# Kernel tuning notes

Measured on AMD Instinct MI355X. Metric: run time of the kernel, lower is better.

## Reference

```python
import jax, jax.numpy as jnp
import numpy as np

INPUT_DIM = 512
LATENT_DIM = 64
H1, H2 = 128, 64  # hardcoded hidden widths in Encoder/Decoder
BATCH = 4096


def _xavier(key, shape):
    fan_out, fan_in = shape
    std = jnp.sqrt(2.0 / (fan_in + fan_out))
    return std * jax.random.normal(key, shape, dtype=jnp.float32)


def setup_inputs() -> dict:
    key = jax.random.key(0)
    ks = jax.random.split(key, 10)
    d = LATENT_DIM
    n_pairs = d * (d - 1) // 2
    n_funcs = 1 + d + n_pairs  # bias + states + pairwise products
    inp = {
        "x": jax.random.normal(ks[0], (BATCH, INPUT_DIM), dtype=jnp.float32),
        "xdot": jax.random.normal(ks[1], (BATCH, INPUT_DIM), dtype=jnp.float32),
        # encoder weights (torch Linear layout: [out, in])
        "We1": _xavier(ks[2], (H1, INPUT_DIM)), "be1": jnp.zeros((H1,), jnp.float32),
        "We2": _xavier(ks[3], (H2, H1)),        "be2": jnp.zeros((H2,), jnp.float32),
        "We3": _xavier(ks[4], (d, H2)),         "be3": jnp.zeros((d,), jnp.float32),
        # decoder weights
        "Wd1": _xavier(ks[5], (H2, d)),         "bd1": jnp.zeros((H2,), jnp.float32),
        "Wd2": _xavier(ks[6], (H1, H2)),        "bd2": jnp.zeros((H1,), jnp.float32),
        "Wd3": _xavier(ks[7], (INPUT_DIM, H1)), "bd3": jnp.zeros((INPUT_DIM,), jnp.float32),
        "XI": jnp.ones((n_funcs, d), jnp.float32),
        "XI_mask": jnp.ones((n_funcs, d), jnp.float32),
    }
    return inp


def _mlp_with_jacobian(x, Ws, bs):
    """3-layer relu MLP; returns output and per-sample analytic Jacobian [B,out,in].
    Jacobian = diag(m3) W3 diag(m2) W2 diag(m1) W1 with relu masks m_l."""
    h = x
    J = None
    for W, b in zip(Ws, bs):
        h = h @ W.T + b                      # [B, out_l]
        m = (h > 0).astype(h.dtype)          # relu mask (grad 0 at 0, matching torch)
        h = jnp.maximum(h, 0)
        Wm = m[:, :, None] * W[None]         # [B, out_l, in_l]
        J = Wm if J is None else jnp.einsum('boh,bhi->boi', Wm, J)
    return h, J


def _sindy_library(z):
    B, d = z.shape
    iu, ju = np.triu_indices(d, k=1)
    ones = jnp.ones((B, 1), z.dtype)
    pairs = z[:, iu] * z[:, ju]              # [B, d(d-1)/2]
    return jnp.concatenate([ones, z, pairs], axis=1)


def reference(x, xdot, We1, be1, We2, be2, We3, be3,
              Wd1, bd1, Wd2, bd2, Wd3, bd3, XI, XI_mask):
    z, Jenc = _mlp_with_jacobian(x, (We1, We2, We3), (be1, be2, be3))
    dz_dt = jnp.einsum('bli,bi->bl', Jenc, xdot)
    xh, Jdec = _mlp_with_jacobian(z, (Wd1, Wd2, Wd3), (bd1, bd2, bd3))
    theta = _sindy_library(z)
    dz_dt_sindy = theta @ (XI_mask * XI)
    dxh_dt = jnp.einsum('bol,bl->bo', Jdec, dz_dt_sindy)
    return (xh, dxh_dt, z, dz_dt, dz_dt_sindy)
```

## Files before the change

kernel.cpp:

```cpp
#include <hip/hip_runtime.h>

#define BATCH 4096
#define IN_DIM 512
#define H1DIM 128
#define H2DIM 64
#define DDIM 64
#define NFUNC 2081
#define NFPAD 2112
#define CHUNK 704
#define KS_PER_CHUNK 22

typedef short bf16x8 __attribute__((ext_vector_type(8)));
typedef float f32x4 __attribute__((ext_vector_type(4)));
#define MFMA(a,b,c) __builtin_amdgcn_mfma_f32_16x16x32_bf16(a,b,c,0,0,0)

#define WSZ1 (H1DIM*IN_DIM)
#define WSZ2 (H2DIM*H1DIM)
#define WSZ3 (DDIM*H2DIM)
#define WSZ4 (H2DIM*DDIM)
#define WSZ5 (H1DIM*H2DIM)
#define WSZ6 (IN_DIM*H1DIM)

__device__ __forceinline__ short f2b(float f) {
    union { float f; unsigned u; } x; x.f = f;
    unsigned r = x.u + 0x7fffu + ((x.u >> 16) & 1u);
    return (short)(r >> 16);
}
__device__ __forceinline__ float b2f(short s) {
    union { unsigned u; float f; } x; x.u = ((unsigned)(unsigned short)s) << 16;
    return x.f;
}
__device__ __forceinline__ void split3f(float v, short& s0, short& s1, short& s2) {
    s0 = f2b(v); float r = v - b2f(s0);
    s1 = f2b(r); float r2 = r - b2f(s1);
    s2 = f2b(r2);
}

__device__ __forceinline__ void st_b16(short* t, int RS, int r, int c, short v) {
    int b = (c * 2) ^ ((r & 7) << 4);
    *(short*)((char*)(t + r * RS) + b) = v;
}
__device__ __forceinline__ void st_b32s(short* t, int RS, int r, int c, unsigned v) {
    int b = (c * 2) ^ ((r & 7) << 4);
    *(unsigned*)((char*)(t + r * RS) + b) = v;
}
__device__ __forceinline__ bf16x8 ld_af(const short* t, int RS, int lane, int kbase) {
    int r = lane & 15;
    int b = ((kbase + (lane >> 4) * 8) * 2) ^ ((r & 7) << 4);
    return *(const bf16x8*)((const char*)(t + r * RS) + b);
}
__device__ __forceinline__ bf16x8 ld_bp(const short* P, int blk, int lane) {
    return *(const bf16x8*)(P + ((size_t)blk * 64 + lane) * 8);
}

__device__ __forceinline__ void mf9(bf16x8 f0, bf16x8 f1, bf16x8 f2, bf16x8 fv,
                                    bf16x8 b0, bf16x8 b1, bf16x8 b2,
                                    f32x4& P, f32x4& Q, f32x4& V) {
    P = MFMA(f0, b0, P); Q = MFMA(f1, b1, Q);
    P = MFMA(f1, b0, P); Q = MFMA(f0, b1, Q);
    P = MFMA(f2, b0, P); Q = MFMA(f2, b1, Q);
    P = MFMA(f0, b2, P); Q = MFMA(f1, b2, Q);
    V = MFMA(fv, b0, V);
}

__device__ __forceinline__ void epi_store(short* t0, short* t1, short* t2, short* tv, int RS,
                                          int lane, int col, const f32x4& P, const f32x4& Q,
                                          const f32x4& V, float bb)
{
    #pragma unroll
    for (int q = 0; q < 4; ++q) {
        int row = (lane >> 4) * 4 + q;
        float pre = P[q] + Q[q] + bb;
        float h = fmaxf(pre, 0.f);
        short s0, s1, s2;
        split3f(h, s0, s1, s2);
        st_b16(t0, RS, row, col, s0);
        st_b16(t1, RS, row, col, s1);
        st_b16(t2, RS, row, col, s2);
        st_b16(tv, RS, row, col, pre > 0.f ? f2b(V[q]) : (short)0);
    }
}

template<int K>
__device__ void pack_w(const float* __restrict__ W, short* __restrict__ dst, int NK,
                       int gid, int nthr)
{
    for (int o = gid; o < NK / 8; o += nthr) {
        int c = o / (K / 8), k0 = (o - c * (K / 8)) * 8;
        int cb = c >> 4, ks = k0 >> 5;
        int L = (((k0 >> 3) & 3) << 4) | (c & 15);
        int idx = ((cb * (K / 32) + ks) * 64 + L) * 8;
        union { short s[8]; bf16x8 v; } p0, p1, p2;
        #pragma unroll
        for (int j = 0; j < 8; ++j)
            split3f(W[(size_t)c * K + k0 + j], p0.s[j], p1.s[j], p2.s[j]);
        *(bf16x8*)(dst + idx) = p0.v;
        *(bf16x8*)(dst + NK + idx) = p1.v;
        *(bf16x8*)(dst + 2 * NK + idx) = p2.v;
    }
}

__global__ void initk(const float* __restrict__ x, const float* __restrict__ xdot,
                      const float* __restrict__ We1, const float* __restrict__ We2,
                      const float* __restrict__ We3, const float* __restrict__ Wd1,
                      const float* __restrict__ Wd2, const float* __restrict__ Wd3,
                      const float* __restrict__ XI, const float* __restrict__ XIm,
                      float* __restrict__ xh, float* __restrict__ dxh,
                      short* Wp1, short* Wp2, short* Wp3, short* Wp4, short* Wp5, short* Wp6,
                      short* xiP, int2* pk)
{
    int gid = blockIdx.x * blockDim.x + threadIdx.x;
    int nthr = gridDim.x * blockDim.x;

    for (int i = gid; i < (BATCH / 16) * 16 * 64; i += nthr) {
        int L = i & 63, ks = (i >> 6) & 15, rb = i >> 10;
        int row = rb * 16 + (L & 15);
        int k0 = ks * 32 + ((L >> 4) << 3);
        const float* px = &x[(size_t)row * IN_DIM + k0];
        const float* pd = &xdot[(size_t)row * IN_DIM + k0];
        f32x4 xa = *(const f32x4*)px, xb = *(const f32x4*)(px + 4);
        f32x4 da = *(const f32x4*)pd, db = *(const f32x4*)(pd + 4);
        union { short s[8]; bf16x8 v; } a0, a1, a2, dv;
        #pragma unroll
        for (int j = 0; j < 4; ++j) {
            split3f(xa[j], a0.s[j], a1.s[j], a2.s[j]);
            split3f(xb[j], a0.s[j + 4], a1.s[j + 4], a2.s[j + 4]);
            dv.s[j] = f2b(da[j]); dv.s[j + 4] = f2b(db[j]);
        }
        short* bx = (short*)(xh + (size_t)rb * 8192);
        short* bd = (short*)(dxh + (size_t)rb * 8192);
        int off = (ks * 64 + L) * 8;
        *(bf16x8*)(bx + off) = a0.v;
        *(bf16x8*)(bx + 8192 + off) = a1.v;
        *(bf16x8*)(bd + off) = a2.v;
        *(bf16x8*)(bd + 8192 + off) = dv.v;
    }

    pack_w<512>(We1, Wp1, WSZ1, gid, nthr);
    pack_w<128>(We2, Wp2, WSZ2, gid, nthr);
    pack_w<64>(We3, Wp3, WSZ3, gid, nthr);
    pack_w<64>(Wd1, Wp4, WSZ4, gid, nthr);
    pack_w<64>(Wd2, Wp5, WSZ5, gid, nthr);
    pack_w<128>(Wd3, Wp6, WSZ6, gid, nthr);

    for (int i = gid; i < 4 * 66 * 64; i += nthr) {
        int cb = i / (66 * 64);
        int r = i - cb * (66 * 64);
        int ks = r >> 6, L = r & 63;
        int col = cb * 16 + (L & 15);
        union { short s[8]; bf16x8 v; } w;
        #pragma unroll
        for (int j = 0; j < 8; ++j) {
            int f = ks * 32 + ((L >> 4) << 3) + j;
            float v = (f < NFUNC) ? XI[(size_t)f * DDIM + col] * XIm[(size_t)f * DDIM + col] : 0.f;
            w.s[j] = f2b(v);
        }
        *(bf16x8*)(xiP + (size_t)i * 8) = w.v;
    }

    for (int f = gid; f < NFPAD; f += nthr) {
        int a, b;
        if (f == 0) { a = 64; b = 64; }
        else if (f <= DDIM) { a = f - 1; b = 64; }
        else if (f < NFUNC) {
            int p = f - 1 - DDIM; int i2 = 0, cum = 0;
            while (cum + (63 - i2) <= p) { cum += 63 - i2; ++i2; }
            a = i2; b = i2 + 1 + (p - cum);
        } else { a = 65; b = 65; }
        pk[f] = make_int2(a, b);
    }
}

__global__ __launch_bounds__(512, 2)
void fused(const float* __restrict__ be1, const float* __restrict__ be2,
           const float* __restrict__ be3, const float* __restrict__ bd1,
           const float* __restrict__ bd2, const float* __restrict__ bd3,
           const short* __restrict__ Wp1, const short* __restrict__ Wp2,
           const short* __restrict__ Wp3, const short* __restrict__ Wp4,
           const short* __restrict__ Wp5, const short* __restrict__ Wp6,
           const short* __restrict__ xiP, const int2* __restrict__ pk,
           float* __restrict__ xh, float* __restrict__ dxh, float* __restrict__ zo,
           float* __restrict__ dz, float* __restrict__ dzs)
{
    __shared__ __align__(16) char ldsbuf[37120];
    short* h1s0 = (short*)(ldsbuf + 0);
    short* h1s1 = (short*)(ldsbuf + 4096);
    short* h1s2 = (short*)(ldsbuf + 8192);
    short* v1   = (short*)(ldsbuf + 12288);
    short* h2s0 = (short*)(ldsbuf + 16384);
    short* h2s1 = (short*)(ldsbuf + 18432);
    short* h2s2 = (short*)(ldsbuf + 20480);
    short* v2   = (short*)(ldsbuf + 22528);
    short* th   = (short*)(ldsbuf + 0);
    short* g1s0 = (short*)(ldsbuf + 0);
    short* g1s1 = (short*)(ldsbuf + 2048);
    short* g1s2 = (short*)(ldsbuf + 4096);
    short* u1   = (short*)(ldsbuf + 6144);
    short* g2s0 = (short*)(ldsbuf + 8192);
    short* g2s1 = (short*)(ldsbuf + 12288);
    short* g2s2 = (short*)(ldsbuf + 16384);
    short* u2   = (short*)(ldsbuf + 20480);
    short* zb0  = (short*)(ldsbuf + 24576);
    short* zb1  = (short*)(ldsbuf + 26624);
    short* zb2  = (short*)(ldsbuf + 28672);
    short* dzsb = (short*)(ldsbuf + 30720);
    float* zf   = (float*)(ldsbuf + 32768);

    const int tid = threadIdx.x, lane = tid & 63, wave = tid >> 6;
    const int wq = wave & 3;
    const int row0 = blockIdx.x * 16;
    const int c16 = lane & 15;
    const int tr = tid & 15, bg = tid >> 4;
    const int tf = bg * 22;

    float bb1 = be1[wave * 16 + c16];
    float bb2 = be2[wq * 16 + c16];
    float bb3 = be3[wq * 16 + c16];
    float bD1 = bd1[wq * 16 + c16];
    float bD2 = bd2[wave * 16 + c16];
    float bD3[4];
    #pragma unroll
    for (int i = 0; i < 4; ++i) bD3[i] = bd3[wave * 64 + i * 16 + c16];

    {
        const short* bx = (const short*)(xh + (size_t)blockIdx.x * 8192);
        const short* bd = (const short*)(dxh + (size_t)blockIdx.x * 8192);
        f32x4 P = {}, Q = {}, V = {};
        bf16x8 A0[3], A1[3], A2[3], Ad[3], B0[3], B1[3], B2[3];
#define L1_LA(ks, sl) { int off = ((ks) * 64 + lane) * 8; \
        A0[sl] = *(const bf16x8*)(bx + off); A1[sl] = *(const bf16x8*)(bx + 8192 + off); \
        A2[sl] = *(const bf16x8*)(bd + off); Ad[sl] = *(const bf16x8*)(bd + 8192 + off); }
#define L1_LB(ks, sl) { int blk = wave * 16 + (ks); \
        B0[sl] = ld_bp(Wp1, blk, lane); B1[sl] = ld_bp(Wp1 + WSZ1, blk, lane); \
        B2[sl] = ld_bp(Wp1 + 2 * WSZ1, blk, lane); }
        L1_LA(0, 0) L1_LB(0, 0)
        L1_LA(1, 1) L1_LB(1, 1)
        L1_LA(2, 2) L1_LB(2, 2)
        #pragma unroll
        for (int ks = 0; ks < 16; ++ks) {
            const int sl = ks % 3;
            mf9(A0[sl], A1[sl], A2[sl], Ad[sl], B0[sl], B1[sl], B2[sl], P, Q, V);
            if (ks + 3 < 16) { L1_LA(ks + 3, sl) L1_LB(ks + 3, sl) }
        }
#undef L1_LA
#undef L1_LB
        epi_store(h1s0, h1s1, h1s2, v1, 128, lane, wave * 16 + c16, P, Q, V, bb1);
    }
    bf16x8 L2B[4][3];
    if (wave < 4) {
        #pragma unroll
        for (int ks = 0; ks < 4; ++ks) {
            int blk = wq * 4 + ks;
            L2B[ks][0] = ld_bp(Wp2, blk, lane);
            L2B[ks][1] = ld_bp(Wp2 + WSZ2, blk, lane);
            L2B[ks][2] = ld_bp(Wp2 + 2 * WSZ2, blk, lane);
        }
    }
    __syncthreads();

    bf16x8 L3B[2][3];
    if (wave < 4) {
        bf16x8 Aa[4][4];
        #pragma unroll
        for (int ks = 0; ks < 4; ++ks) {
            Aa[ks][0] = ld_af(h1s0, 128, lane, ks * 32);
            Aa[ks][1] = ld_af(h1s1, 128, lane, ks * 32);
            Aa[ks][2] = ld_af(h1s2, 128, lane, ks * 32);
            Aa[ks][3] = ld_af(v1, 128, lane, ks * 32);
        }
        #pragma unroll
        for (int ks = 0; ks < 2; ++ks) {
            int blk = wq * 2 + ks;
            L3B[ks][0] = ld_bp(Wp3, blk, lane);
            L3B[ks][1] = ld_bp(Wp3 + WSZ3, blk, lane);
            L3B[ks][2] = ld_bp(Wp3 + 2 * WSZ3, blk, lane);
        }
        f32x4 P = {}, Q = {}, V = {};
        #pragma unroll
        for (int ks = 0; ks < 4; ++ks)
            mf9(Aa[ks][0], Aa[ks][1], Aa[ks][2], Aa[ks][3], L2B[ks][0], L2B[ks][1], L2B[ks][2], P, Q, V);
        epi_store(h2s0, h2s1, h2s2, v2, 64, lane, wq * 16 + c16, P, Q, V, bb2);
    }
    __syncthreads();

    bf16x8 X[KS_PER_CHUNK];
    if (wave < 4) {
        bf16x8 Aa[2][4];
        #pragma unroll
        for (int ks = 0; ks < 2; ++ks) {
            Aa[ks][0] = ld_af(h2s0, 64, lane, ks * 32);
            Aa[ks][1] = ld_af(h2s1, 64, lane, ks * 32);
            Aa[ks][2] = ld_af(h2s2, 64, lane, ks * 32);
            Aa[ks][3] = ld_af(v2, 64, lane, ks * 32);
        }
        f32x4 P = {}, Q = {}, V = {};
        #pragma unroll
        for (int ks = 0; ks < 2; ++ks)
            mf9(Aa[ks][0], Aa[ks][1], Aa[ks][2], Aa[ks][3], L3B[ks][0], L3B[ks][1], L3B[ks][2], P, Q, V);
        #pragma unroll
        for (int kk = 0; kk < KS_PER_CHUNK; ++kk)
            X[kk] = ld_bp(xiP, wq * 66 + kk, lane);
        int col = wq * 16 + c16;
        #pragma unroll
        for (int q = 0; q < 4; ++q) {
            int row = (lane >> 4) * 4 + q;
            float pre = P[q] + Q[q] + bb3;
            float hz = fmaxf(pre, 0.f);
            float vz = pre > 0.f ? V[q] : 0.f;
            zf[row * 68 + col] = hz;
            short s0, s1, s2;
            split3f(hz, s0, s1, s2);
            st_b16(zb0, 64, row, col, s0);
            st_b16(zb1, 64, row, col, s1);
            st_b16(zb2, 64, row, col, s2);
            zo[(size_t)(row0 + row) * DDIM + col] = hz;
            dz[(size_t)(row0 + row) * DDIM + col] = vz;
        }
        if (tid < 32) { int r = tid & 15; zf[r * 68 + 64 + (tid >> 4)] = (tid >> 4) ? 0.f : 1.f; }
    }
    __syncthreads();

    f32x4 sa0 = {}, sa1 = {};
    auto build = [&](int ch) {
        #pragma clang loop unroll(disable)
        for (int j = 0; j < 11; ++j) {
            int f0 = ch * CHUNK + tf + 2 * j;
            int2 p0 = pk[f0], p1 = pk[f0 + 1];
            float t0 = zf[tr * 68 + p0.x] * zf[tr * 68 + p0.y];
            float t1 = zf[tr * 68 + p1.x] * zf[tr * 68 + p1.y];
            unsigned u = (unsigned)(unsigned short)f2b(t0)
                       | ((unsigned)(unsigned short)f2b(t1) << 16);
            st_b32s(th, 704, tr, tf + 2 * j, u);
        }
    };
#define SMF() { _Pragma("unroll") for (int kk = 0; kk < KS_PER_CHUNK; ++kk) { \
        bf16x8 a = ld_af(th, 704, lane, kk * 32); \
        if (kk & 1) sa1 = MFMA(a, X[kk], sa1); else sa0 = MFMA(a, X[kk], sa0); } }
#define ISX(ch) { _Pragma("unroll") for (int kk = 0; kk < KS_PER_CHUNK; ++kk) \
        X[kk] = ld_bp(xiP, wq * 66 + (ch) * KS_PER_CHUNK + kk, lane); }

    build(0);
    __syncthreads();
    if (wave < 4) { SMF() ISX(1) }
    __syncthreads();
    build(1);
    __syncthreads();
    if (wave < 4) { SMF() ISX(2) }
    __syncthreads();
    build(2);
    __syncthreads();
    bf16x8 D1B[2][3];
    if (wave < 4) {
        SMF()
        f32x4 sacc = sa0 + sa1;
        #pragma unroll
        for (int ks = 0; ks < 2; ++ks) {
            int blk = wq * 2 + ks;
            D1B[ks][0] = ld_bp(Wp4, blk, lane);
            D1B[ks][1] = ld_bp(Wp4 + WSZ4, blk, lane);
            D1B[ks][2] = ld_bp(Wp4 + 2 * WSZ4, blk, lane);
        }
        int col = wq * 16 + c16;
        #pragma unroll
        for (int q = 0; q < 4; ++q) {
            int row = (lane >> 4) * 4 + q;
            float v = sacc[q];
            dzs[(size_t)(row0 + row) * DDIM + col] = v;
            st_b16(dzsb, 64, row, col, f2b(v));
        }
    }
#undef SMF
#undef ISX
    __syncthreads();

    bf16x8 D2B[2][3];
    if (wave < 4) {
        bf16x8 Aa[2][4];
        #pragma unroll
        for (int ks = 0; ks < 2; ++ks) {
            Aa[ks][0] = ld_af(zb0, 64, lane, ks * 32);
            Aa[ks][1] = ld_af(zb1, 64, lane, ks * 32);
            Aa[ks][2] = ld_af(zb2, 64, lane, ks * 32);
            Aa[ks][3] = ld_af(dzsb, 64, lane, ks * 32);
        }
        f32x4 P = {}, Q = {}, V = {};
        #pragma unroll
        for (int ks = 0; ks < 2; ++ks)
            mf9(Aa[ks][0], Aa[ks][1], Aa[ks][2], Aa[ks][3], D1B[ks][0], D1B[ks][1], D1B[ks][2], P, Q, V);
        epi_store(g1s0, g1s1, g1s2, u1, 64, lane, wq * 16 + c16, P, Q, V, bD1);
    }
    #pragma unroll
    for (int ks = 0; ks < 2; ++ks) {
        int blk = wave * 2 + ks;
        D2B[ks][0] = ld_bp(Wp5, blk, lane);
        D2B[ks][1] = ld_bp(Wp5 + WSZ5, blk, lane);
        D2B[ks][2] = ld_bp(Wp5 + 2 * WSZ5, blk, lane);
    }
    __syncthreads();

    {
        bf16x8 Aa[2][4];
        #pragma unroll
        for (int ks = 0; ks < 2; ++ks) {
            Aa[ks][0] = ld_af(g1s0, 64, lane, ks * 32);
            Aa[ks][1] = ld_af(g1s1, 64, lane, ks * 32);
            Aa[ks][2] = ld_af(g1s2, 64, lane, ks * 32);
            Aa[ks][3] = ld_af(u1, 64, lane, ks * 32);
        }
        f32x4 P = {}, Q = {}, V = {};
        #pragma unroll
        for (int ks = 0; ks < 2; ++ks)
            mf9(Aa[ks][0], Aa[ks][1], Aa[ks][2], Aa[ks][3], D2B[ks][0], D2B[ks][1], D2B[ks][2], P, Q, V);
        epi_store(g2s0, g2s1, g2s2, u2, 128, lane, wave * 16 + c16, P, Q, V, bD2);
    }
    __syncthreads();

    {
        f32x4 P[4] = {}, Q[4] = {}, V[4] = {};
        bf16x8 Bp[4][3];
        bf16x8 Ax0[2], Ax1[2], Ax2[2], Axv[2];
#define D3_LA(ks, b) { Ax0[b] = ld_af(g2s0, 128, lane, (ks) * 32); Ax1[b] = ld_af(g2s1, 128, lane, (ks) * 32); \
                       Ax2[b] = ld_af(g2s2, 128, lane, (ks) * 32); Axv[b] = ld_af(u2, 128, lane, (ks) * 32); }
#define D3_LB(s, sl) { int blk = (wave * 4 + ((s) & 3)) * 4 + ((s) >> 2); \
        Bp[sl][0] = ld_bp(Wp6, blk, lane); Bp[sl][1] = ld_bp(Wp6 + WSZ6, blk, lane); \
        Bp[sl][2] = ld_bp(Wp6 + 2 * WSZ6, blk, lane); }
        D3_LA(0, 0)
        D3_LB(0, 0) D3_LB(1, 1) D3_LB(2, 2) D3_LB(3, 3)
        #pragma unroll
        for (int ks = 0; ks < 4; ++ks) {
            if (ks < 3) D3_LA(ks + 1, (ks + 1) & 1)
            #pragma unroll
            for (int cf = 0; cf < 4; ++cf) {
                const int s = ks * 4 + cf, sl = s & 3;
                mf9(Ax0[ks & 1], Ax1[ks & 1], Ax2[ks & 1], Axv[ks & 1],
                    Bp[sl][0], Bp[sl][1], Bp[sl][2], P[cf], Q[cf], V[cf]);
                if (s + 4 < 16) D3_LB(s + 4, sl)
            }
        }
#undef D3_LA
#undef D3_LB
        #pragma unroll
        for (int cf = 0; cf < 4; ++cf) {
            int col = wave * 64 + cf * 16 + c16;
            float bb = bD3[cf];
            #pragma unroll
            for (int q = 0; q < 4; ++q) {
                int row = (lane >> 4) * 4 + q;
                float pre = P[cf][q] + Q[cf][q] + bb;
                xh[(size_t)(row0 + row) * IN_DIM + col] = fmaxf(pre, 0.f);
                dxh[(size_t)(row0 + row) * IN_DIM + col] = pre > 0.f ? V[cf][q] : 0.f;
            }
        }
    }
}

extern "C" void kernel_launch(void* const* d_in, const int* in_sizes, int n_in,
                              void* d_out, int out_size, void* d_ws, size_t ws_size,
                              hipStream_t stream)
{
    const float* x    = (const float*)d_in[0];
    const float* xdot = (const float*)d_in[1];
    const float* We1  = (const float*)d_in[2];
    const float* be1  = (const float*)d_in[3];
    const float* We2  = (const float*)d_in[4];
    const float* be2  = (const float*)d_in[5];
    const float* We3  = (const float*)d_in[6];
    const float* be3  = (const float*)d_in[7];
    const float* Wd1  = (const float*)d_in[8];
    const float* bd1  = (const float*)d_in[9];
    const float* Wd2  = (const float*)d_in[10];
    const float* bd2  = (const float*)d_in[11];
    const float* Wd3  = (const float*)d_in[12];
    const float* bd3  = (const float*)d_in[13];
    const float* XI   = (const float*)d_in[14];
    const float* XIm  = (const float*)d_in[15];

    float* out = (float*)d_out;
    float* xh  = out;
    float* dxh = out + (size_t)BATCH * IN_DIM;
    float* zo  = dxh + (size_t)BATCH * IN_DIM;
    float* dz  = zo + (size_t)BATCH * DDIM;
    float* dzs = dz + (size_t)BATCH * DDIM;

    int2*  pk  = (int2*)d_ws;
    short* Wp1 = (short*)(pk + NFPAD);
    short* Wp2 = Wp1 + 3 * WSZ1;
    short* Wp3 = Wp2 + 3 * WSZ2;
    short* Wp4 = Wp3 + 3 * WSZ3;
    short* Wp5 = Wp4 + 3 * WSZ4;
    short* Wp6 = Wp5 + 3 * WSZ5;
    short* xiP = Wp6 + 3 * WSZ6;

    initk<<<1024, 256, 0, stream>>>(x, xdot, We1, We2, We3, Wd1, Wd2, Wd3, XI, XIm,
                                    xh, dxh, Wp1, Wp2, Wp3, Wp4, Wp5, Wp6, xiP, pk);
    fused<<<BATCH / 16, 512, 0, stream>>>(be1, be2, be3, bd1, bd2, bd3,
                                          Wp1, Wp2, Wp3, Wp4, Wp5, Wp6, xiP, pk,
                                          xh, dxh, zo, dz, dzs);
}
```

Measured before the change: 50.19 us.

## Double block size to 16 waves, split layer-1 K across wave halves

The fused kernel now launches 1024 threads per block instead of 512, so each 16-row tile is handled by 16 waves. Layer 1 splits its K dimension between two wave halves and sums the partial accumulators through a new LDS reduction buffer. The decoder's last layer gives each wave half as many output columns, and the SINDy library build now has each thread write one bf16 term at a time. The aim is more parallelism and latency hiding per tile, at the cost of a larger LDS footprint, an extra barrier and reduction, idle waves in some stages, and the removal of the explicit software prefetch in the final layer.

```diff
diff --git a/kernel.cpp b/kernel.cpp
--- a/kernel.cpp
+++ b/kernel.cpp
@@ -39,10 +39,6 @@
 __device__ __forceinline__ void st_b16(short* t, int RS, int r, int c, short v) {
     int b = (c * 2) ^ ((r & 7) << 4);
     *(short*)((char*)(t + r * RS) + b) = v;
-}
-__device__ __forceinline__ void st_b32s(short* t, int RS, int r, int c, unsigned v) {
-    int b = (c * 2) ^ ((r & 7) << 4);
-    *(unsigned*)((char*)(t + r * RS) + b) = v;
 }
 __device__ __forceinline__ bf16x8 ld_af(const short* t, int RS, int lane, int kbase) {
     int r = lane & 15;
@@ -171,7 +167,7 @@
     }
 }
 
-__global__ __launch_bounds__(512, 2)
+__global__ __launch_bounds__(1024, 4)
 void fused(const float* __restrict__ be1, const float* __restrict__ be2,
            const float* __restrict__ be3, const float* __restrict__ bd1,
            const float* __restrict__ bd2, const float* __restrict__ bd3,
@@ -182,7 +178,7 @@
            float* __restrict__ xh, float* __restrict__ dxh, float* __restrict__ zo,
            float* __restrict__ dz, float* __restrict__ dzs)
 {
-    __shared__ __align__(16) char ldsbuf[37120];
+    __shared__ __align__(16) char ldsbuf[49152];
     short* h1s0 = (short*)(ldsbuf + 0);
     short* h1s1 = (short*)(ldsbuf + 4096);
     short* h1s2 = (short*)(ldsbuf + 8192);
@@ -205,46 +201,59 @@
     short* zb2  = (short*)(ldsbuf + 28672);
     short* dzsb = (short*)(ldsbuf + 30720);
     float* zf   = (float*)(ldsbuf + 32768);
+    float* rbuf = (float*)(ldsbuf + 16384);
 
     const int tid = threadIdx.x, lane = tid & 63, wave = tid >> 6;
     const int wq = wave & 3;
     const int row0 = blockIdx.x * 16;
     const int c16 = lane & 15;
     const int tr = tid & 15, bg = tid >> 4;
-    const int tf = bg * 22;
-
-    float bb1 = be1[wave * 16 + c16];
+
+    const int cb1 = wave & 7, kh1 = wave >> 3;
+    float bb1 = be1[cb1 * 16 + c16];
     float bb2 = be2[wq * 16 + c16];
     float bb3 = be3[wq * 16 + c16];
     float bD1 = bd1[wq * 16 + c16];
-    float bD2 = bd2[wave * 16 + c16];
-    float bD3[4];
+    float bD2 = (wave < 8) ? bd2[wave * 16 + c16] : 0.f;
+    float bD3[2];
     #pragma unroll
-    for (int i = 0; i < 4; ++i) bD3[i] = bd3[wave * 64 + i * 16 + c16];
+    for (int i = 0; i < 2; ++i) bD3[i] = bd3[wave * 32 + i * 16 + c16];
 
     {
         const short* bx = (const short*)(xh + (size_t)blockIdx.x * 8192);
         const short* bd = (const short*)(dxh + (size_t)blockIdx.x * 8192);
+        const int ksb = kh1 * 8;
         f32x4 P = {}, Q = {}, V = {};
         bf16x8 A0[3], A1[3], A2[3], Ad[3], B0[3], B1[3], B2[3];
-#define L1_LA(ks, sl) { int off = ((ks) * 64 + lane) * 8; \
+#define L1_LA(ks, sl) { int off = ((ksb + (ks)) * 64 + lane) * 8; \
         A0[sl] = *(const bf16x8*)(bx + off); A1[sl] = *(const bf16x8*)(bx + 8192 + off); \
         A2[sl] = *(const bf16x8*)(bd + off); Ad[sl] = *(const bf16x8*)(bd + 8192 + off); }
-#define L1_LB(ks, sl) { int blk = wave * 16 + (ks); \
+#define L1_LB(ks, sl) { int blk = cb1 * 16 + ksb + (ks); \
         B0[sl] = ld_bp(Wp1, blk, lane); B1[sl] = ld_bp(Wp1 + WSZ1, blk, lane); \
         B2[sl] = ld_bp(Wp1 + 2 * WSZ1, blk, lane); }
         L1_LA(0, 0) L1_LB(0, 0)
         L1_LA(1, 1) L1_LB(1, 1)
         L1_LA(2, 2) L1_LB(2, 2)
         #pragma unroll
-        for (int ks = 0; ks < 16; ++ks) {
+        for (int ks = 0; ks < 8; ++ks) {
             const int sl = ks % 3;
             mf9(A0[sl], A1[sl], A2[sl], Ad[sl], B0[sl], B1[sl], B2[sl], P, Q, V);
-            if (ks + 3 < 16) { L1_LA(ks + 3, sl) L1_LB(ks + 3, sl) }
+            if (ks + 3 < 8) { L1_LA(ks + 3, sl) L1_LB(ks + 3, sl) }
         }
 #undef L1_LA
 #undef L1_LB
-        epi_store(h1s0, h1s1, h1s2, v1, 128, lane, wave * 16 + c16, P, Q, V, bb1);
+        if (kh1 == 1) {
+            float* rb = rbuf + (cb1 * 64 + lane) * 16;
+            *(f32x4*)(rb + 0) = P; *(f32x4*)(rb + 4) = Q; *(f32x4*)(rb + 8) = V;
+        }
+        __syncthreads();
+        if (kh1 == 0) {
+            const float* rb = rbuf + (cb1 * 64 + lane) * 16;
+            f32x4 P2 = P + *(const f32x4*)(rb + 0);
+            f32x4 Q2 = Q + *(const f32x4*)(rb + 4);
+            f32x4 V2 = V + *(const f32x4*)(rb + 8);
+            epi_store(h1s0, h1s1, h1s2, v1, 128, lane, cb1 * 16 + c16, P2, Q2, V2, bb1);
+        }
     }
     bf16x8 L2B[4][3];
     if (wave < 4) {
@@ -324,13 +333,10 @@
     auto build = [&](int ch) {
         #pragma clang loop unroll(disable)
         for (int j = 0; j < 11; ++j) {
-            int f0 = ch * CHUNK + tf + 2 * j;
-            int2 p0 = pk[f0], p1 = pk[f0 + 1];
+            int fl = bg * 11 + j;
+            int2 p0 = pk[ch * CHUNK + fl];
             float t0 = zf[tr * 68 + p0.x] * zf[tr * 68 + p0.y];
-            float t1 = zf[tr * 68 + p1.x] * zf[tr * 68 + p1.y];
-            unsigned u = (unsigned)(unsigned short)f2b(t0)
-                       | ((unsigned)(unsigned short)f2b(t1) << 16);
-            st_b32s(th, 704, tr, tf + 2 * j, u);
+            st_b16(th, 704, tr, fl, f2b(t0));
         }
     };
 #define SMF() { _Pragma("unroll") for (int kk = 0; kk < KS_PER_CHUNK; ++kk) { \
@@ -389,16 +395,18 @@
             mf9(Aa[ks][0], Aa[ks][1], Aa[ks][2], Aa[ks][3], D1B[ks][0], D1B[ks][1], D1B[ks][2], P, Q, V);
         epi_store(g1s0, g1s1, g1s2, u1, 64, lane, wq * 16 + c16, P, Q, V, bD1);
     }
-    #pragma unroll
-    for (int ks = 0; ks < 2; ++ks) {
-        int blk = wave * 2 + ks;
-        D2B[ks][0] = ld_bp(Wp5, blk, lane);
-        D2B[ks][1] = ld_bp(Wp5 + WSZ5, blk, lane);
-        D2B[ks][2] = ld_bp(Wp5 + 2 * WSZ5, blk, lane);
-    }
-    __syncthreads();
-
-    {
+    if (wave < 8) {
+        #pragma unroll
+        for (int ks = 0; ks < 2; ++ks) {
+            int blk = wave * 2 + ks;
+            D2B[ks][0] = ld_bp(Wp5, blk, lane);
+            D2B[ks][1] = ld_bp(Wp5 + WSZ5, blk, lane);
+            D2B[ks][2] = ld_bp(Wp5 + 2 * WSZ5, blk, lane);
+        }
+    }
+    __syncthreads();
+
+    if (wave < 8) {
         bf16x8 Aa[2][4];
         #pragma unroll
         for (int ks = 0; ks < 2; ++ks) {
@@ -416,32 +424,25 @@
     __syncthreads();
 
     {
-        f32x4 P[4] = {}, Q[4] = {}, V[4] = {};
-        bf16x8 Bp[4][3];
-        bf16x8 Ax0[2], Ax1[2], Ax2[2], Axv[2];
-#define D3_LA(ks, b) { Ax0[b] = ld_af(g2s0, 128, lane, (ks) * 32); Ax1[b] = ld_af(g2s1, 128, lane, (ks) * 32); \
-                       Ax2[b] = ld_af(g2s2, 128, lane, (ks) * 32); Axv[b] = ld_af(u2, 128, lane, (ks) * 32); }
-#define D3_LB(s, sl) { int blk = (wave * 4 + ((s) & 3)) * 4 + ((s) >> 2); \
-        Bp[sl][0] = ld_bp(Wp6, blk, lane); Bp[sl][1] = ld_bp(Wp6 + WSZ6, blk, lane); \
-        Bp[sl][2] = ld_bp(Wp6 + 2 * WSZ6, blk, lane); }
-        D3_LA(0, 0)
-        D3_LB(0, 0) D3_LB(1, 1) D3_LB(2, 2) D3_LB(3, 3)
-        #pragma unroll
-        for (int ks = 0; ks < 4; ++ks) {
-            if (ks < 3) D3_LA(ks + 1, (ks + 1) & 1)
+        f32x4 P[2] = {}, Q[2] = {}, V[2] = {};
+        #pragma unroll
+        for (int ksc = 0; ksc < 4; ++ksc) {
+            bf16x8 a0 = ld_af(g2s0, 128, lane, ksc * 32);
+            bf16x8 a1 = ld_af(g2s1, 128, lane, ksc * 32);
+            bf16x8 a2 = ld_af(g2s2, 128, lane, ksc * 32);
+            bf16x8 av = ld_af(u2, 128, lane, ksc * 32);
             #pragma unroll
-            for (int cf = 0; cf < 4; ++cf) {
-                const int s = ks * 4 + cf, sl = s & 3;
-                mf9(Ax0[ks & 1], Ax1[ks & 1], Ax2[ks & 1], Axv[ks & 1],
-                    Bp[sl][0], Bp[sl][1], Bp[sl][2], P[cf], Q[cf], V[cf]);
-                if (s + 4 < 16) D3_LB(s + 4, sl)
+            for (int cf = 0; cf < 2; ++cf) {
+                int blk = (wave * 2 + cf) * 4 + ksc;
+                bf16x8 b0 = ld_bp(Wp6, blk, lane);
+                bf16x8 b1 = ld_bp(Wp6 + WSZ6, blk, lane);
+                bf16x8 b2 = ld_bp(Wp6 + 2 * WSZ6, blk, lane);
+                mf9(a0, a1, a2, av, b0, b1, b2, P[cf], Q[cf], V[cf]);
             }
         }
-#undef D3_LA
-#undef D3_LB
-        #pragma unroll
-        for (int cf = 0; cf < 4; ++cf) {
-            int col = wave * 64 + cf * 16 + c16;
+        #pragma unroll
+        for (int cf = 0; cf < 2; ++cf) {
+            int col = wave * 32 + cf * 16 + c16;
             float bb = bD3[cf];
             #pragma unroll
             for (int q = 0; q < 4; ++q) {
@@ -493,7 +494,7 @@
 
     initk<<<1024, 256, 0, stream>>>(x, xdot, We1, We2, We3, Wd1, Wd2, Wd3, XI, XIm,
                                     xh, dxh, Wp1, Wp2, Wp3, Wp4, Wp5, Wp6, xiP, pk);
-    fused<<<BATCH / 16, 512, 0, stream>>>(be1, be2, be3, bd1, bd2, bd3,
-                                          Wp1, Wp2, Wp3, Wp4, Wp5, Wp6, xiP, pk,
-                                          xh, dxh, zo, dz, dzs);
-}
+    fused<<<BATCH / 16, 1024, 0, stream>>>(be1, be2, be3, bd1, bd2, bd3,
+                                           Wp1, Wp2, Wp3, Wp4, Wp5, Wp6, xiP, pk,
+                                           xh, dxh, zo, dz, dzs);
+}
```

Result: no change. 50.33 us (+0.3%).
